# Kernel optimization log

Hardware: AMD Instinct MI355X
Metric: run time of the kernel (lower is better)

## Reference

```python
import jax, jax.numpy as jnp
import numpy as np

B, S, H, NH = 8, 1024, 1024, 16
D = H // NH          # attention_hidden_size = 64
V = S                # v_size must equal seq_len (mask broadcast)


def setup_inputs() -> dict:
    key = jax.random.key(0)
    ks = jax.random.split(key, 9)
    s = 0.02
    return {
        "q": jax.random.normal(ks[0], (B, S, H), jnp.float32),
        "k": jax.random.normal(ks[1], (B, S, H), jnp.float32),
        "v": jax.random.normal(ks[2], (B, S, H), jnp.float32),
        # per-head Q/K projections, stacked over heads: (NH, H, D)
        "Wq": jax.random.normal(ks[3], (NH, H, D), jnp.float32) * s,
        "bq": jax.random.normal(ks[4], (NH, D), jnp.float32) * s,
        "Wk": jax.random.normal(ks[5], (NH, H, D), jnp.float32) * s,
        "bk": jax.random.normal(ks[6], (NH, D), jnp.float32) * s,
        # shared V projection hidden -> v_size
        "Wv": jax.random.normal(ks[7], (H, V), jnp.float32) * s,
        "bv": jax.random.normal(ks[8], (V,), jnp.float32) * s,
    }


def reference(q, k, v, Wq, bq, Wk, bk, Wv, bv):
    d = Wq.shape[-1]
    scale = d ** (-0.5)
    # per-head projections, heads vectorized into leading axis n
    qh = jnp.einsum('bsh,nhd->nbsd', q, Wq) + bq[:, None, None, :]
    kh = jnp.einsum('bth,nhd->nbtd', k, Wk) + bk[:, None, None, :]
    vv = jnp.einsum('bth,hv->btv', v, Wv) + bv          # shared V: (B,S,V)
    seq = q.shape[1]
    mask = jnp.triu(jnp.full((seq, seq), -jnp.inf, dtype=q.dtype), 1)
    scores = jnp.einsum('nbsd,nbtd->nbst', qh, kh) * scale + mask
    p = jax.nn.softmax(scores, axis=-1)                  # (NH,B,S,S)
    # matmul against shared V then mean over heads (== stack + mean)
    out = jnp.einsum('nbst,btv->nbsv', p, vv).mean(axis=0)
    return out
```

## Files before the change

kernel.cpp:

```cpp
#include <hip/hip_runtime.h>


#define NHEAD 16
#define BATCH 8
#define SEQ   1024
#define HID   1024
#define DHEAD 64

typedef _Float16 f16;
typedef _Float16 f16x4 __attribute__((ext_vector_type(4)));
typedef _Float16 f16x8 __attribute__((ext_vector_type(8)));
typedef float    f32x4 __attribute__((ext_vector_type(4)));

__device__ __forceinline__ f32x4 mfma16(f16x8 a, f16x8 b, f32x4 c) {
  return __builtin_amdgcn_mfma_f32_16x16x32_f16(a, b, c, 0, 0, 0);
}

__device__ __forceinline__ void gload16(const f16* g, f16* l) {
  __builtin_amdgcn_global_load_lds(
      (const __attribute__((address_space(1))) void*)g,
      (__attribute__((address_space(3))) void*)l, 16, 0, 0);
}

__device__ __forceinline__ void stage_swz(const f16* __restrict__ g, int ldg,
                                          f16* lds, int nch, int tid) {
  for (int idx = tid; idx < nch; idx += 256) {
    int row = idx >> 3, c16 = idx & 7;
    int sc = c16 ^ (row & 7);
    gload16(g + (size_t)row * ldg + sc * 8, lds + (size_t)(idx & ~63) * 8);
  }
}

__device__ __forceinline__ f16x8 lds_frag(const f16* lds, int row, int c16) {
  int sc = c16 ^ (row & 7);
  return *(const f16x8*)&lds[row * 64 + sc * 8];
}


__global__ __launch_bounds__(256) void conv3(
    const float* __restrict__ q, const float* __restrict__ k,
    const float* __restrict__ v, f16* __restrict__ dq, f16* __restrict__ dk,
    f16* __restrict__ dv) {
  const float* src = blockIdx.z == 0 ? q : blockIdx.z == 1 ? k : v;
  f16* dst = blockIdx.z == 0 ? dq : blockIdx.z == 1 ? dk : dv;
  int i = (blockIdx.x * 256 + threadIdx.x) * 4;
  float4 f = *(const float4*)(src + i);
  f16x4 o = { (f16)f.x, (f16)f.y, (f16)f.z, (f16)f.w };
  *(f16x4*)(dst + i) = o;
}

__global__ __launch_bounds__(256) void tconv2(
    const float* __restrict__ s0, const float* __restrict__ s1,
    f16* __restrict__ d0, f16* __restrict__ d1, int R, int C, int half) {
  int z = blockIdx.z;
  const float* src; f16* dst;
  if (z < half) { src = s0 + (size_t)z * R * C; dst = d0 + (size_t)z * R * C; }
  else { src = s1 + (size_t)(z - half) * R * C; dst = d1 + (size_t)(z - half) * R * C; }
  const int c0 = blockIdx.x * 64, r0 = blockIdx.y * 64;
  __shared__ f16 t[64][72];
  const int tid = threadIdx.x;
#pragma unroll
  for (int i = 0; i < 4; i++) {
    int chunk = tid + i * 256;
    int row = chunk >> 4, c4 = chunk & 15;
    float4 f = *(const float4*)&src[(size_t)(r0 + row) * C + c0 + c4 * 4];
    f16x4 h = { (f16)f.x, (f16)f.y, (f16)f.z, (f16)f.w };
    *(f16x4*)&t[row][c4 * 4] = h;
  }
  __syncthreads();
  const int cc = tid >> 2, q = tid & 3;
  f16 tmp[16];
#pragma unroll
  for (int j = 0; j < 16; j++) tmp[j] = t[q * 16 + j][cc];
  *(f16x8*)&dst[(size_t)(c0 + cc) * R + r0 + q * 16] = *(f16x8*)&tmp[0];
  *(f16x8*)&dst[(size_t)(c0 + cc) * R + r0 + q * 16 + 8] = *(f16x8*)&tmp[8];
}


__device__ __forceinline__ void gemm_core(
    const f16* __restrict__ A, const f16* __restrict__ Bt, int K, int Kend,
    int row0, int col0, f16* la, f16* lb, int tid, f32x4 (&acc)[4][4]) {
  const int lane = tid & 63;
  const int wr = (tid >> 6) >> 1, wc = (tid >> 6) & 1;
  for (int k0 = 0; k0 < Kend; k0 += 64) {
    __syncthreads();
    stage_swz(A + (size_t)row0 * K + k0, K, la, 1024, tid);
    stage_swz(Bt + (size_t)col0 * K + k0, K, lb, 1024, tid);
    __syncthreads();
#pragma unroll
    for (int ks = 0; ks < 2; ks++) {
      f16x8 af[4], bfr[4];
#pragma unroll
      for (int mi = 0; mi < 4; mi++)
        af[mi] = lds_frag(la, wr * 64 + mi * 16 + (lane & 15), ks * 4 + (lane >> 4));
#pragma unroll
      for (int ni = 0; ni < 4; ni++)
        bfr[ni] = lds_frag(lb, wc * 64 + ni * 16 + (lane & 15), ks * 4 + (lane >> 4));
#pragma unroll
      for (int mi = 0; mi < 4; mi++)
#pragma unroll
        for (int ni = 0; ni < 4; ni++)
          acc[mi][ni] = mfma16(af[mi], bfr[ni], acc[mi][ni]);
    }
  }
}


__global__ __launch_bounds__(256) void proj_gemm(
    const f16* __restrict__ A0, const f16* __restrict__ A1,
    const f16* __restrict__ Bt0, const f16* __restrict__ Bt1,
    const float* __restrict__ bias0, const float* __restrict__ bias1,
    f16* __restrict__ C0, f16* __restrict__ C1) {
  const int which = blockIdx.z;
  const f16* A = which ? A1 : A0;
  const f16* Bt = which ? Bt1 : Bt0;
  const float* bias = which ? bias1 : bias0;
  f16* C = which ? C1 : C0;
  __shared__ alignas(16) f16 la[128 * 64];
  __shared__ alignas(16) f16 lb[128 * 64];
  const int tid = threadIdx.x, lane = tid & 63;
  const int wr = (tid >> 6) >> 1, wc = (tid >> 6) & 1;
  const int row0 = blockIdx.x * 128, col0 = blockIdx.y * 128;
  f32x4 acc[4][4];
#pragma unroll
  for (int i = 0; i < 4; i++)
#pragma unroll
    for (int j = 0; j < 4; j++) acc[i][j] = (f32x4){0.f, 0.f, 0.f, 0.f};
  gemm_core(A, Bt, HID, HID, row0, col0, la, lb, tid, acc);
#pragma unroll
  for (int mi = 0; mi < 4; mi++)
#pragma unroll
    for (int ni = 0; ni < 4; ni++)
#pragma unroll
      for (int r = 0; r < 4; r++) {
        int m = row0 + wr * 64 + mi * 16 + ((lane >> 4) << 2) + r;
        int j = col0 + wc * 64 + ni * 16 + (lane & 15);
        float val = acc[mi][ni][r] + bias[j];
        int bb = m >> 10, s = m & 1023, hn = j >> 6, d = j & 63;
        C[(((size_t)hn * BATCH + bb) * SEQ + s) * DHEAD + d] = (f16)val;
      }
}


__global__ __launch_bounds__(256) void vv_gemm(
    const f16* __restrict__ A, const f16* __restrict__ Bt,
    const float* __restrict__ bias, f16* __restrict__ C) {
  __shared__ alignas(16) f16 la[128 * 64];
  __shared__ alignas(16) f16 lb[128 * 64];
  const int tid = threadIdx.x, lane = tid & 63;
  const int wr = (tid >> 6) >> 1, wc = (tid >> 6) & 1;
  const int row0 = blockIdx.x * 128, col0 = blockIdx.y * 128;
  f32x4 acc[4][4];
#pragma unroll
  for (int i = 0; i < 4; i++)
#pragma unroll
    for (int j = 0; j < 4; j++) acc[i][j] = (f32x4){0.f, 0.f, 0.f, 0.f};
  gemm_core(A, Bt, HID, HID, row0, col0, la, lb, tid, acc);
#pragma unroll
  for (int mi = 0; mi < 4; mi++)
#pragma unroll
    for (int ni = 0; ni < 4; ni++)
#pragma unroll
      for (int r = 0; r < 4; r++) {
        int m = row0 + wr * 64 + mi * 16 + ((lane >> 4) << 2) + r;
        int j = col0 + wc * 64 + ni * 16 + (lane & 15);
        float val = acc[mi][ni][r] + bias[m];
        int bb = j >> 10, t = j & 1023;
        C[((size_t)bb * SEQ + m) * SEQ + t] = (f16)val;
      }
}


template <int NTC>
__device__ __forceinline__ void stats_chunk(
    const f16* lkbuf, f16x8 aq0, f16x8 aq1, int lane, int k0, int srow,
    bool masked, float sl2e, float (&l_p)[4]) {
#pragma unroll
  for (int tc = 0; tc < NTC; tc++) {
    f16x8 b0 = lds_frag(lkbuf, tc * 16 + (lane & 15), (lane >> 4));
    f16x8 b1 = lds_frag(lkbuf, tc * 16 + (lane & 15), 4 + (lane >> 4));
    f32x4 c = (f32x4){0.f, 0.f, 0.f, 0.f};
    c = mfma16(aq0, b0, c);
    c = mfma16(aq1, b1, c);
    int tg = k0 + tc * 16 + (lane & 15);
#pragma unroll
    for (int r = 0; r < 4; r++) {
      float e = exp2f(c[r] * sl2e);
      if (masked) e = (tg <= srow + r) ? e : 0.f;
      l_p[r] += e;
    }
  }
}

__global__ __launch_bounds__(256) void attn_stats(
    const f16* __restrict__ QH, const f16* __restrict__ KH,
    float* __restrict__ madj_ws) {
  const int sb = 15 - blockIdx.x;
  const int b = blockIdx.y, n = blockIdx.z;
  const int s0 = sb * 64;
  const f16* qh = QH + ((size_t)n * BATCH + b) * SEQ * DHEAD;
  const f16* kh = KH + ((size_t)n * BATCH + b) * SEQ * DHEAD;

  __shared__ alignas(16) f16 lq[64 * 64];
  __shared__ alignas(16) f16 lk[2][256 * 64];

  const int tid = threadIdx.x, lane = tid & 63, wave = tid >> 6;
  const int KROWS = s0 + 64;
  const int nsteps = (sb + 4) >> 2;

  stage_swz(qh + (size_t)s0 * 64, 64, lq, 512, tid);
  {
    int rows0 = KROWS < 256 ? KROWS : 256;
    stage_swz(kh, 64, lk[0], rows0 * 8, tid);
  }
  __syncthreads();

  f16x8 aq0 = lds_frag(lq, wave * 16 + (lane & 15), (lane >> 4));
  f16x8 aq1 = lds_frag(lq, wave * 16 + (lane & 15), 4 + (lane >> 4));

  const float sl2e = 0.125f * 1.44269504088896f;
  float l_p[4] = {0.f, 0.f, 0.f, 0.f};
  const int srow = s0 + wave * 16 + ((lane >> 4) << 2);

  int cur = 0;
  for (int st = 0; st < nsteps; st++) {
    int k0 = st << 8;
    int rows = KROWS - k0; if (rows > 256) rows = 256;
    if (st + 1 < nsteps) {
      int rows1 = KROWS - (k0 + 256); if (rows1 > 256) rows1 = 256;
      stage_swz(kh + (size_t)(k0 + 256) * 64, 64, lk[cur ^ 1], rows1 * 8, tid);
    }
    bool last = (st == nsteps - 1);
    if (rows == 256)      stats_chunk<16>(lk[cur], aq0, aq1, lane, k0, srow, last, sl2e, l_p);
    else if (rows == 192) stats_chunk<12>(lk[cur], aq0, aq1, lane, k0, srow, last, sl2e, l_p);
    else if (rows == 128) stats_chunk<8>(lk[cur], aq0, aq1, lane, k0, srow, last, sl2e, l_p);
    else                  stats_chunk<4>(lk[cur], aq0, aq1, lane, k0, srow, last, sl2e, l_p);
    __syncthreads();
    cur ^= 1;
  }

#pragma unroll
  for (int r = 0; r < 4; r++) {
    float l = l_p[r];
#pragma unroll
    for (int off = 1; off < 16; off <<= 1) l += __shfl_xor(l, off);
    if ((lane & 15) == 0) {
      size_t base = ((size_t)n * BATCH + b) * SEQ;
      madj_ws[base + srow + r] = -__log2f(l) - 4.0f;
    }
  }
}


__global__ __launch_bounds__(256) void attn_pbar(
    const f16* __restrict__ QH, const f16* __restrict__ KH,
    const float* __restrict__ madj_ws, f16* __restrict__ pp) {
  int f = blockIdx.x, sb = 0, tcid = 0;
  for (int s = 15; s >= 0; --s) {
    int c = (s >> 2) + 1;
    if (f < c) { sb = s; tcid = f; break; }
    f -= c;
  }
  const int s0 = sb * 64, t0 = tcid * 256;
  const int b = blockIdx.y >> 1, g = blockIdx.y & 1;

  __shared__ alignas(16) f16 lq[2][64 * 64];
  __shared__ alignas(16) f16 lk[2][256 * 64];

  const int tid = threadIdx.x, lane = tid & 63, wave = tid >> 6;
  const float sl2e = 0.125f * 1.44269504088896f;
  const int srow = s0 + wave * 16 + ((lane >> 4) << 2);
  const int n0 = g * 8;
  const int ntc_act = ((s0 + 63 - t0) >> 4) + 1 < 16 ? ((s0 + 63 - t0) >> 4) + 1 : 16;

  float pacc[16][4];
#pragma unroll
  for (int tc = 0; tc < 16; tc++)
#pragma unroll
    for (int r = 0; r < 4; r++) pacc[tc][r] = 0.f;

  stage_swz(QH + ((size_t)n0 * BATCH + b) * SEQ * DHEAD + (size_t)s0 * 64, 64,
            lq[0], 512, tid);
  stage_swz(KH + ((size_t)n0 * BATCH + b) * SEQ * DHEAD + (size_t)t0 * 64, 64,
            lk[0], 2048, tid);
  __syncthreads();

  int cur = 0;
  for (int nn = 0; nn < 8; nn++) {
    const int n = n0 + nn;
    if (nn + 1 < 8) {
      const f16* qh1 = QH + ((size_t)(n + 1) * BATCH + b) * SEQ * DHEAD;
      const f16* kh1 = KH + ((size_t)(n + 1) * BATCH + b) * SEQ * DHEAD;
      stage_swz(qh1 + (size_t)s0 * 64, 64, lq[cur ^ 1], 512, tid);
      stage_swz(kh1 + (size_t)t0 * 64, 64, lk[cur ^ 1], 2048, tid);
    }

    f16x8 aq0 = lds_frag(lq[cur], wave * 16 + (lane & 15), (lane >> 4));
    f16x8 aq1 = lds_frag(lq[cur], wave * 16 + (lane & 15), 4 + (lane >> 4));

    float4 ma = *(const float4*)&madj_ws[((size_t)n * BATCH + b) * SEQ + srow];
    float madj[4] = {ma.x, ma.y, ma.z, ma.w};

#pragma unroll
    for (int tc = 0; tc < 16; tc++) {
      if (tc < ntc_act) {
        f16x8 b0 = lds_frag(lk[cur], tc * 16 + (lane & 15), (lane >> 4));
        f16x8 b1 = lds_frag(lk[cur], tc * 16 + (lane & 15), 4 + (lane >> 4));
        f32x4 c = (f32x4){0.f, 0.f, 0.f, 0.f};
        c = mfma16(aq0, b0, c);
        c = mfma16(aq1, b1, c);
        int tg = t0 + tc * 16 + (lane & 15);
        bool edge = (t0 + tc * 16 + 15) > s0;
#pragma unroll
        for (int r = 0; r < 4; r++) {
          float p = exp2f(fmaf(c[r], sl2e, madj[r]));
          if (edge) p = (tg <= srow + r) ? p : 0.f;
          pacc[tc][r] += p;
        }
      }
    }
    __syncthreads();
    cur ^= 1;
  }

  f16* out = pp + ((size_t)g * BATCH + b) * SEQ * SEQ;
#pragma unroll
  for (int tc = 0; tc < 16; tc++) {
    int tg = t0 + tc * 16 + (lane & 15);
#pragma unroll
    for (int r = 0; r < 4; r++)
      out[(size_t)(srow + r) * SEQ + tg] = (f16)pacc[tc][r];
  }
}


__global__ __launch_bounds__(256) void pv_gemm(
    const f16* __restrict__ pp, const f16* __restrict__ vvT,
    float* __restrict__ out) {
  const int b = blockIdx.z;
  const size_t GS = (size_t)BATCH * SEQ * SEQ;
  const f16* A0 = pp + (size_t)b * SEQ * SEQ;
  const f16* A1 = pp + GS + (size_t)b * SEQ * SEQ;
  const f16* Bt = vvT + (size_t)b * SEQ * SEQ;
  __shared__ alignas(16) f16 la0[128 * 64];
  __shared__ alignas(16) f16 la1[128 * 64];
  __shared__ alignas(16) f16 lb[128 * 64];
  const int tid = threadIdx.x, lane = tid & 63;
  const int wr = (tid >> 6) >> 1, wc = (tid >> 6) & 1;
  const int row0 = blockIdx.x * 128, col0 = blockIdx.y * 128;
  const int Kend = (row0 + 128 < SEQ) ? row0 + 128 : SEQ;

  f32x4 acc[4][4];
#pragma unroll
  for (int i = 0; i < 4; i++)
#pragma unroll
    for (int j = 0; j < 4; j++) acc[i][j] = (f32x4){0.f, 0.f, 0.f, 0.f};

  for (int k0 = 0; k0 < Kend; k0 += 64) {
    __syncthreads();
    stage_swz(A0 + (size_t)row0 * SEQ + k0, SEQ, la0, 1024, tid);
    stage_swz(A1 + (size_t)row0 * SEQ + k0, SEQ, la1, 1024, tid);
    stage_swz(Bt + (size_t)col0 * SEQ + k0, SEQ, lb, 1024, tid);
    __syncthreads();
#pragma unroll
    for (int ks = 0; ks < 2; ks++) {
      f16x8 a0[4], a1[4], bfr[4];
#pragma unroll
      for (int mi = 0; mi < 4; mi++) {
        a0[mi] = lds_frag(la0, wr * 64 + mi * 16 + (lane & 15), ks * 4 + (lane >> 4));
        a1[mi] = lds_frag(la1, wr * 64 + mi * 16 + (lane & 15), ks * 4 + (lane >> 4));
      }
#pragma unroll
      for (int ni = 0; ni < 4; ni++)
        bfr[ni] = lds_frag(lb, wc * 64 + ni * 16 + (lane & 15), ks * 4 + (lane >> 4));
#pragma unroll
      for (int mi = 0; mi < 4; mi++)
#pragma unroll
        for (int ni = 0; ni < 4; ni++) {
          acc[mi][ni] = mfma16(a0[mi], bfr[ni], acc[mi][ni]);
          acc[mi][ni] = mfma16(a1[mi], bfr[ni], acc[mi][ni]);
        }
    }
  }

#pragma unroll
  for (int mi = 0; mi < 4; mi++)
#pragma unroll
    for (int ni = 0; ni < 4; ni++)
#pragma unroll
      for (int r = 0; r < 4; r++) {
        int m = row0 + wr * 64 + mi * 16 + ((lane >> 4) << 2) + r;
        int j = col0 + wc * 64 + ni * 16 + (lane & 15);
        out[(size_t)b * SEQ * SEQ + (size_t)m * SEQ + j] = acc[mi][ni][r];
      }
}


extern "C" void kernel_launch(void* const* d_in, const int* in_sizes, int n_in,
                              void* d_out, int out_size, void* d_ws, size_t ws_size,
                              hipStream_t stream) {
  (void)in_sizes; (void)n_in; (void)out_size; (void)ws_size;
  const float* q  = (const float*)d_in[0];
  const float* k  = (const float*)d_in[1];
  const float* v  = (const float*)d_in[2];
  const float* Wq = (const float*)d_in[3];
  const float* bq = (const float*)d_in[4];
  const float* Wk = (const float*)d_in[5];
  const float* bk = (const float*)d_in[6];
  const float* Wv = (const float*)d_in[7];
  const float* bv = (const float*)d_in[8];
  float* out = (float*)d_out;

  const size_t EL  = (size_t)BATCH * SEQ * HID;
  const size_t WEL = (size_t)NHEAD * HID * DHEAD;

  char* ws = (char*)d_ws;
  f16* qbf = (f16*)ws;  ws += EL * 2;
  f16* kbf = (f16*)ws;  ws += EL * 2;
  f16* vbf = (f16*)ws;  ws += EL * 2;
  f16* WqT = (f16*)ws;  ws += WEL * 2;
  f16* WkT = (f16*)ws;  ws += WEL * 2;
  f16* WvT = (f16*)ws;  ws += WEL * 2;
  f16* QHb = (f16*)ws;  ws += EL * 2;
  f16* KHb = (f16*)ws;  ws += EL * 2;
  f16* vvT = (f16*)ws;  ws += EL * 2;
  float* madj_ws = (float*)ws; ws += (size_t)NHEAD * BATCH * SEQ * 4;
  f16* pp = qbf;

  conv3<<<dim3(8192, 1, 3), 256, 0, stream>>>(q, k, v, qbf, kbf, vbf);
  tconv2<<<dim3(1, 16, 32), 256, 0, stream>>>(Wq, Wk, WqT, WkT, 1024, 64, 16);
  tconv2<<<dim3(16, 16, 1), 256, 0, stream>>>(Wv, Wv, WvT, WvT, 1024, 1024, 1);

  proj_gemm<<<dim3(64, 8, 2), 256, 0, stream>>>(qbf, kbf, WqT, WkT, bq, bk,
                                                QHb, KHb);
  vv_gemm<<<dim3(8, 64, 1), 256, 0, stream>>>(WvT, vbf, bv, vvT);

  attn_stats<<<dim3(16, 8, 16), 256, 0, stream>>>(QHb, KHb, madj_ws);
  attn_pbar<<<dim3(40, 16, 1), 256, 0, stream>>>(QHb, KHb, madj_ws, pp);
  pv_gemm<<<dim3(8, 8, 8), 256, 0, stream>>>(pp, vvT, out);
}
```

Before: 272.5 us.

## Load Q/K MFMA fragments directly from global memory, shrink pbar tiles

Measured after the change: 338.5 us. 1.24x slower.

```diff
diff --git a/kernel.cpp b/kernel.cpp
--- a/kernel.cpp
+++ b/kernel.cpp
@@ -171,27 +171,6 @@
 }
 
 
-template <int NTC>
-__device__ __forceinline__ void stats_chunk(
-    const f16* lkbuf, f16x8 aq0, f16x8 aq1, int lane, int k0, int srow,
-    bool masked, float sl2e, float (&l_p)[4]) {
-#pragma unroll
-  for (int tc = 0; tc < NTC; tc++) {
-    f16x8 b0 = lds_frag(lkbuf, tc * 16 + (lane & 15), (lane >> 4));
-    f16x8 b1 = lds_frag(lkbuf, tc * 16 + (lane & 15), 4 + (lane >> 4));
-    f32x4 c = (f32x4){0.f, 0.f, 0.f, 0.f};
-    c = mfma16(aq0, b0, c);
-    c = mfma16(aq1, b1, c);
-    int tg = k0 + tc * 16 + (lane & 15);
-#pragma unroll
-    for (int r = 0; r < 4; r++) {
-      float e = exp2f(c[r] * sl2e);
-      if (masked) e = (tg <= srow + r) ? e : 0.f;
-      l_p[r] += e;
-    }
-  }
-}
-
 __global__ __launch_bounds__(256) void attn_stats(
     const f16* __restrict__ QH, const f16* __restrict__ KH,
     float* __restrict__ madj_ws) {
@@ -201,42 +180,54 @@
   const f16* qh = QH + ((size_t)n * BATCH + b) * SEQ * DHEAD;
   const f16* kh = KH + ((size_t)n * BATCH + b) * SEQ * DHEAD;
 
-  __shared__ alignas(16) f16 lq[64 * 64];
-  __shared__ alignas(16) f16 lk[2][256 * 64];
-
   const int tid = threadIdx.x, lane = tid & 63, wave = tid >> 6;
-  const int KROWS = s0 + 64;
-  const int nsteps = (sb + 4) >> 2;
-
-  stage_swz(qh + (size_t)s0 * 64, 64, lq, 512, tid);
-  {
-    int rows0 = KROWS < 256 ? KROWS : 256;
-    stage_swz(kh, 64, lk[0], rows0 * 8, tid);
-  }
-  __syncthreads();
-
-  f16x8 aq0 = lds_frag(lq, wave * 16 + (lane & 15), (lane >> 4));
-  f16x8 aq1 = lds_frag(lq, wave * 16 + (lane & 15), 4 + (lane >> 4));
+  const int qrow = s0 + wave * 16 + (lane & 15);
+  const int ch = (lane >> 4) << 3;
+
+  f16x8 aq0 = *(const f16x8*)&qh[(size_t)qrow * 64 + ch];
+  f16x8 aq1 = *(const f16x8*)&qh[(size_t)qrow * 64 + 32 + ch];
 
   const float sl2e = 0.125f * 1.44269504088896f;
   float l_p[4] = {0.f, 0.f, 0.f, 0.f};
   const int srow = s0 + wave * 16 + ((lane >> 4) << 2);
-
-  int cur = 0;
-  for (int st = 0; st < nsteps; st++) {
-    int k0 = st << 8;
-    int rows = KROWS - k0; if (rows > 256) rows = 256;
-    if (st + 1 < nsteps) {
-      int rows1 = KROWS - (k0 + 256); if (rows1 > 256) rows1 = 256;
-      stage_swz(kh + (size_t)(k0 + 256) * 64, 64, lk[cur ^ 1], rows1 * 8, tid);
-    }
-    bool last = (st == nsteps - 1);
-    if (rows == 256)      stats_chunk<16>(lk[cur], aq0, aq1, lane, k0, srow, last, sl2e, l_p);
-    else if (rows == 192) stats_chunk<12>(lk[cur], aq0, aq1, lane, k0, srow, last, sl2e, l_p);
-    else if (rows == 128) stats_chunk<8>(lk[cur], aq0, aq1, lane, k0, srow, last, sl2e, l_p);
-    else                  stats_chunk<4>(lk[cur], aq0, aq1, lane, k0, srow, last, sl2e, l_p);
-    __syncthreads();
-    cur ^= 1;
+  const int nf = (s0 >> 4) + wave;
+
+  const f16* kp = kh + (size_t)(lane & 15) * 64 + ch;
+  int t = 0;
+  for (; t + 2 <= nf; t += 2) {
+    const f16* p = kp + (size_t)t * 1024;
+    f16x8 b0a = *(const f16x8*)(p);
+    f16x8 b1a = *(const f16x8*)(p + 32);
+    f16x8 b0b = *(const f16x8*)(p + 1024);
+    f16x8 b1b = *(const f16x8*)(p + 1024 + 32);
+    f32x4 ca = (f32x4){0.f, 0.f, 0.f, 0.f};
+    f32x4 cb = (f32x4){0.f, 0.f, 0.f, 0.f};
+    ca = mfma16(aq0, b0a, ca); ca = mfma16(aq1, b1a, ca);
+    cb = mfma16(aq0, b0b, cb); cb = mfma16(aq1, b1b, cb);
+#pragma unroll
+    for (int r = 0; r < 4; r++)
+      l_p[r] += exp2f(ca[r] * sl2e) + exp2f(cb[r] * sl2e);
+  }
+  if (t < nf) {
+    const f16* p = kp + (size_t)t * 1024;
+    f16x8 b0 = *(const f16x8*)(p);
+    f16x8 b1 = *(const f16x8*)(p + 32);
+    f32x4 c = (f32x4){0.f, 0.f, 0.f, 0.f};
+    c = mfma16(aq0, b0, c); c = mfma16(aq1, b1, c);
+#pragma unroll
+    for (int r = 0; r < 4; r++) l_p[r] += exp2f(c[r] * sl2e);
+    t++;
+  }
+  {
+    const f16* p = kp + (size_t)nf * 1024;
+    f16x8 b0 = *(const f16x8*)(p);
+    f16x8 b1 = *(const f16x8*)(p + 32);
+    f32x4 c = (f32x4){0.f, 0.f, 0.f, 0.f};
+    c = mfma16(aq0, b0, c); c = mfma16(aq1, b1, c);
+    int tg = (nf << 4) + (lane & 15);
+#pragma unroll
+    for (int r = 0; r < 4; r++)
+      l_p[r] += (tg <= srow + r) ? exp2f(c[r] * sl2e) : 0.f;
   }
 
 #pragma unroll
@@ -257,75 +248,63 @@
     const float* __restrict__ madj_ws, f16* __restrict__ pp) {
   int f = blockIdx.x, sb = 0, tcid = 0;
   for (int s = 15; s >= 0; --s) {
-    int c = (s >> 2) + 1;
+    int c = (s >> 1) + 1;
     if (f < c) { sb = s; tcid = f; break; }
     f -= c;
   }
-  const int s0 = sb * 64, t0 = tcid * 256;
+  const int s0 = sb * 64, t0 = tcid * 128;
   const int b = blockIdx.y >> 1, g = blockIdx.y & 1;
-
-  __shared__ alignas(16) f16 lq[2][64 * 64];
-  __shared__ alignas(16) f16 lk[2][256 * 64];
+  const int n0 = g * 8;
 
   const int tid = threadIdx.x, lane = tid & 63, wave = tid >> 6;
   const float sl2e = 0.125f * 1.44269504088896f;
+  const int ch = (lane >> 4) << 3;
+  const int qrow = s0 + wave * 16 + (lane & 15);
   const int srow = s0 + wave * 16 + ((lane >> 4) << 2);
-  const int n0 = g * 8;
-  const int ntc_act = ((s0 + 63 - t0) >> 4) + 1 < 16 ? ((s0 + 63 - t0) >> 4) + 1 : 16;
-
-  float pacc[16][4];
-#pragma unroll
-  for (int tc = 0; tc < 16; tc++)
+  const int wmin = s0 + wave * 16;
+  int ntc = ((wmin + 15 - t0) >> 4) + 1;
+  ntc = ntc < 0 ? 0 : (ntc > 8 ? 8 : ntc);
+
+  float pacc[8][4];
+#pragma unroll
+  for (int tc = 0; tc < 8; tc++)
 #pragma unroll
     for (int r = 0; r < 4; r++) pacc[tc][r] = 0.f;
 
-  stage_swz(QH + ((size_t)n0 * BATCH + b) * SEQ * DHEAD + (size_t)s0 * 64, 64,
-            lq[0], 512, tid);
-  stage_swz(KH + ((size_t)n0 * BATCH + b) * SEQ * DHEAD + (size_t)t0 * 64, 64,
-            lk[0], 2048, tid);
-  __syncthreads();
-
-  int cur = 0;
   for (int nn = 0; nn < 8; nn++) {
     const int n = n0 + nn;
-    if (nn + 1 < 8) {
-      const f16* qh1 = QH + ((size_t)(n + 1) * BATCH + b) * SEQ * DHEAD;
-      const f16* kh1 = KH + ((size_t)(n + 1) * BATCH + b) * SEQ * DHEAD;
-      stage_swz(qh1 + (size_t)s0 * 64, 64, lq[cur ^ 1], 512, tid);
-      stage_swz(kh1 + (size_t)t0 * 64, 64, lk[cur ^ 1], 2048, tid);
-    }
-
-    f16x8 aq0 = lds_frag(lq[cur], wave * 16 + (lane & 15), (lane >> 4));
-    f16x8 aq1 = lds_frag(lq[cur], wave * 16 + (lane & 15), 4 + (lane >> 4));
-
+    const f16* qh = QH + ((size_t)n * BATCH + b) * SEQ * DHEAD;
+    const f16* kh = KH + ((size_t)n * BATCH + b) * SEQ * DHEAD;
+    f16x8 aq0 = *(const f16x8*)&qh[(size_t)qrow * 64 + ch];
+    f16x8 aq1 = *(const f16x8*)&qh[(size_t)qrow * 64 + 32 + ch];
     float4 ma = *(const float4*)&madj_ws[((size_t)n * BATCH + b) * SEQ + srow];
     float madj[4] = {ma.x, ma.y, ma.z, ma.w};
-
-#pragma unroll
-    for (int tc = 0; tc < 16; tc++) {
-      if (tc < ntc_act) {
-        f16x8 b0 = lds_frag(lk[cur], tc * 16 + (lane & 15), (lane >> 4));
-        f16x8 b1 = lds_frag(lk[cur], tc * 16 + (lane & 15), 4 + (lane >> 4));
+    const f16* kp = kh + (size_t)(t0 + (lane & 15)) * 64 + ch;
+
+#pragma unroll
+    for (int tc = 0; tc < 8; tc++) {
+      if (tc < ntc) {
+        const f16* p = kp + (size_t)tc * 1024;
+        f16x8 b0 = *(const f16x8*)(p);
+        f16x8 b1 = *(const f16x8*)(p + 32);
         f32x4 c = (f32x4){0.f, 0.f, 0.f, 0.f};
         c = mfma16(aq0, b0, c);
         c = mfma16(aq1, b1, c);
         int tg = t0 + tc * 16 + (lane & 15);
-        bool edge = (t0 + tc * 16 + 15) > s0;
+        bool edge = (t0 + tc * 16 + 15) > wmin;
 #pragma unroll
         for (int r = 0; r < 4; r++) {
-          float p = exp2f(fmaf(c[r], sl2e, madj[r]));
-          if (edge) p = (tg <= srow + r) ? p : 0.f;
-          pacc[tc][r] += p;
+          float p2 = exp2f(fmaf(c[r], sl2e, madj[r]));
+          if (edge) p2 = (tg <= srow + r) ? p2 : 0.f;
+          pacc[tc][r] += p2;
         }
       }
     }
-    __syncthreads();
-    cur ^= 1;
   }
 
   f16* out = pp + ((size_t)g * BATCH + b) * SEQ * SEQ;
 #pragma unroll
-  for (int tc = 0; tc < 16; tc++) {
+  for (int tc = 0; tc < 8; tc++) {
     int tg = t0 + tc * 16 + (lane & 15);
 #pragma unroll
     for (int r = 0; r < 4; r++)
@@ -436,6 +415,6 @@
   vv_gemm<<<dim3(8, 64, 1), 256, 0, stream>>>(WvT, vbf, bv, vvT);
 
   attn_stats<<<dim3(16, 8, 16), 256, 0, stream>>>(QHb, KHb, madj_ws);
-  attn_pbar<<<dim3(40, 16, 1), 256, 0, stream>>>(QHb, KHb, madj_ws, pp);
+  attn_pbar<<<dim3(72, 16, 1), 256, 0, stream>>>(QHb, KHb, madj_ws, pp);
   pv_gemm<<<dim3(8, 8, 8), 256, 0, stream>>>(pp, vvT, out);
 }
```
